# Kernel optimization log

Measured on AMD Instinct MI355X. Metric: run time of the kernel, lower is better.

## Reference

```python
import math
import jax, jax.numpy as jnp
import numpy as np

VOCAB = 50257
HIDDEN = 768
TYPE_VOCAB = 2
MAX_POS = 5000
EPS = 1e-12


def sinusoidal_pe(max_len, dim):
    # matches SinPositionalEncoding: pe[:,0::2]=sin(pos*div), pe[:,1::2]=cos(pos*div)
    position = np.arange(max_len, dtype=np.float32)[:, None]
    div_term = np.exp(np.arange(0, dim, 2, dtype=np.float32) * -(math.log(10000.0) / dim))
    pe = np.zeros((max_len, dim), dtype=np.float32)
    pe[:, 0::2] = np.sin(position * div_term)
    pe[:, 1::2] = np.cos(position * div_term)
    return jnp.asarray(pe)  # [max_len, dim]


def setup_inputs() -> dict:
    key = jax.random.key(0)
    k1, k2, k3, k4, k5 = jax.random.split(key, 5)
    B, N = 8, 4096
    return {
        "input_ids": jax.random.randint(k1, (B, N), 0, VOCAB, dtype=jnp.int64 if jax.config.jax_enable_x64 else jnp.int32),
        "tok_struct_vec": jax.random.randint(k2, (B, N, 3), 0, MAX_POS, dtype=jnp.int32),
        "token_type_ids": jax.random.randint(k3, (B, N), 0, TYPE_VOCAB, dtype=jnp.int32),
        "word_emb": jax.random.normal(k4, (VOCAB, HIDDEN), dtype=jnp.float32) * 0.02,
        "type_emb": jax.random.normal(k5, (TYPE_VOCAB, HIDDEN), dtype=jnp.float32) * 0.02,
        "gamma": jnp.ones((HIDDEN,), dtype=jnp.float32),
        "beta": jnp.zeros((HIDDEN,), dtype=jnp.float32),
    }


def reference(input_ids, tok_struct_vec, token_type_ids, word_emb, type_emb, gamma, beta):
    B, N = input_ids.shape
    pe = sinusoidal_pe(MAX_POS, HIDDEN)  # [max_pos, H]

    words = word_emb[input_ids]                      # [B,N,H] gather
    types = type_emb[token_type_ids]                 # [B,N,H] gather
    pos = jnp.broadcast_to(pe[:N][None], (B, N, HIDDEN))  # pe[:, :n].expand

    # compute_se: vectorized gather of pe rows by structure positions
    para = pe[tok_struct_vec[:, :, 0]]               # [B,N,H]
    sent = pe[tok_struct_vec[:, :, 1]]
    tok = pe[tok_struct_vec[:, :, 2]]
    struct = para + sent + tok                       # tok_se_comb_mode == 'sum'

    emb = words + pos + types + struct
    # BertLayerNorm (eps=1e-12); dropout is identity in eval
    mean = jnp.mean(emb, axis=-1, keepdims=True)
    var = jnp.mean(jnp.square(emb - mean), axis=-1, keepdims=True)
    out = (emb - mean) / jnp.sqrt(var + EPS) * gamma + beta
    return out
```

## Files before the change

kernel.cpp:

```cpp
#include <hip/hip_runtime.h>
#include <hip/hip_fp16.h>
#include <cstdint>
#include <cmath>

#define HIDDEN   768
#define NPAIR    (HIDDEN / 2)
#define SEQ_N    4096
#define LN_EPS   1e-12f
#define N_HI     80
#define N_LO     64
#define NBLK     2048

typedef float    f4v __attribute__((ext_vector_type(4)));
typedef _Float16 h4v __attribute__((ext_vector_type(4)));

__global__ __launch_bounds__(256) void pe_tables_kernel(__half2* __restrict__ T) {
    const int total = (N_HI + N_LO) * NPAIR;
    int idx = blockIdx.x * 256 + threadIdx.x;
    if (idx >= total) return;
    int r = idx / NPAIR;
    int i = idx % NPAIR;
    const float L = logf(10000.0f) / (float)HIDDEN;
    float div = expf(-2.0f * (float)i * L);
    int p = (r < N_HI) ? (r << 6) : (r - N_HI);
    float s, c;
    sincosf((float)p * div, &s, &c);
    T[idx] = __floats2half2_rn(s, c);
}

__device__ __forceinline__ void pe_acc(float4& x, const h4v a, const h4v b) {
    const float sA0 = (float)a.x, cA0 = (float)a.y, sA1 = (float)a.z, cA1 = (float)a.w;
    const float sB0 = (float)b.x, cB0 = (float)b.y, sB1 = (float)b.z, cB1 = (float)b.w;
    x.x = fmaf(sA0, cB0, fmaf(cA0, sB0, x.x));
    x.y = fmaf(cA0, cB0, fmaf(-sA0, sB0, x.y));
    x.z = fmaf(sA1, cB1, fmaf(cA1, sB1, x.z));
    x.w = fmaf(cA1, cB1, fmaf(-sA1, sB1, x.w));
}

__global__ __launch_bounds__(256, 4) void emb_ln_kernel(
    const int*     __restrict__ ids,
    const int*     __restrict__ svec,
    const int*     __restrict__ tt,
    const float*   __restrict__ word_emb,
    const float*   __restrict__ type_emb,
    const float*   __restrict__ gamma,
    const float*   __restrict__ beta,
    const __half2* __restrict__ T,
    float*         __restrict__ out,
    int n_tokens)
{
    const int wave = threadIdx.x >> 6;
    const int lane = threadIdx.x & 63;
    const int nw   = NBLK * 4;
    int tok = blockIdx.x * 4 + wave;
    if (tok >= n_tokens) return;

    int tu = __builtin_amdgcn_readfirstlane(tok);
    int id = ids[tu], ty = tt[tu];
    int p0 = svec[3 * tu], p1 = svec[3 * tu + 1], p2 = svec[3 * tu + 2];

    for (;;) {
        const int n = tu & (SEQ_N - 1);

        const float4* wrow = reinterpret_cast<const float4*>(word_emb + (size_t)id * HIDDEN);
        const float4* trow = reinterpret_cast<const float4*>(type_emb + (size_t)ty * HIDDEN);

        #define T1ROW(p) reinterpret_cast<const h4v*>(T + (size_t)((p) >> 6) * NPAIR)
        #define T2ROW(p) reinterpret_cast<const h4v*>(T + (size_t)(N_HI + ((p) & 63)) * NPAIR)
        const h4v* A0 = T1ROW(n),  *B0 = T2ROW(n);
        const h4v* A1 = T1ROW(p0), *B1 = T2ROW(p0);
        const h4v* A2 = T1ROW(p1), *B2 = T2ROW(p1);
        const h4v* A3 = T1ROW(p2), *B3 = T2ROW(p2);
        #undef T1ROW
        #undef T2ROW

        const int tnext = tu + nw;
        const bool more = tnext < n_tokens;
        int id_n = 0, ty_n = 0, q0 = 0, q1 = 0, q2 = 0;
        if (more) {
            id_n = ids[tnext]; ty_n = tt[tnext];
            q0 = svec[3 * tnext]; q1 = svec[3 * tnext + 1]; q2 = svec[3 * tnext + 2];
        }

        float4 acc[3];
        float s = 0.0f, ss = 0.0f;

        #pragma unroll
        for (int k = 0; k < 3; ++k) {
            const int d4 = lane + 64 * k;

            float4 w = wrow[d4];
            float4 t = trow[d4];
            h4v a0 = A0[d4], b0 = B0[d4];
            h4v a1 = A1[d4], b1 = B1[d4];
            h4v a2 = A2[d4], b2 = B2[d4];
            h4v a3 = A3[d4], b3 = B3[d4];

            float4 x;
            x.x = w.x + t.x; x.y = w.y + t.y; x.z = w.z + t.z; x.w = w.w + t.w;
            pe_acc(x, a0, b0);
            pe_acc(x, a1, b1);
            pe_acc(x, a2, b2);
            pe_acc(x, a3, b3);

            acc[k] = x;
            s  += x.x + x.y + x.z + x.w;
            ss += x.x * x.x + x.y * x.y + x.z * x.z + x.w * x.w;
        }

        #pragma unroll
        for (int off = 1; off < 64; off <<= 1) {
            s  += __shfl_xor(s,  off);
            ss += __shfl_xor(ss, off);
        }

        const float mean = s * (1.0f / (float)HIDDEN);
        const float var  = ss * (1.0f / (float)HIDDEN) - mean * mean;
        const float inv  = rsqrtf(var + LN_EPS);

        const float4* g4 = reinterpret_cast<const float4*>(gamma);
        const float4* b4 = reinterpret_cast<const float4*>(beta);
        float4* orow = reinterpret_cast<float4*>(out + (size_t)tu * HIDDEN);

        #pragma unroll
        for (int k = 0; k < 3; ++k) {
            const int d4 = lane + 64 * k;
            const float4 g = g4[d4];
            const float4 b = b4[d4];
            const float4 x = acc[k];
            float4 r;
            r.x = (x.x - mean) * inv * g.x + b.x;
            r.y = (x.y - mean) * inv * g.y + b.y;
            r.z = (x.z - mean) * inv * g.z + b.z;
            r.w = (x.w - mean) * inv * g.w + b.w;
            orow[d4] = r;
        }

        if (!more) break;
        tu = tnext; id = id_n; ty = ty_n; p0 = q0; p1 = q1; p2 = q2;
    }
}

extern "C" void kernel_launch(void* const* d_in, const int* in_sizes, int n_in,
                              void* d_out, int out_size, void* d_ws, size_t ws_size,
                              hipStream_t stream) {
    const int*   ids      = (const int*)d_in[0];
    const int*   svec     = (const int*)d_in[1];
    const int*   tt       = (const int*)d_in[2];
    const float* word_emb = (const float*)d_in[3];
    const float* type_emb = (const float*)d_in[4];
    const float* gamma    = (const float*)d_in[5];
    const float* beta     = (const float*)d_in[6];
    float*       out      = (float*)d_out;

    const int n_tokens = in_sizes[0];

    __half2* T = (__half2*)d_ws;
    const int total_tab = (N_HI + N_LO) * NPAIR;
    pe_tables_kernel<<<(total_tab + 255) / 256, 256, 0, stream>>>(T);
    emb_ln_kernel<<<NBLK, 256, 0, stream>>>(
        ids, svec, tt, word_emb, type_emb, gamma, beta, T, out, n_tokens);
}
```

Baseline: 51.34 us.

## Software-pipeline word-embedding row loads and use nontemporal output stores

Each wave now prefetches the next token's word-embedding row into registers while it computes the current token, and it fetches the indices two tokens ahead. The aim is to hide the latency of the random gathers from the large word table. The output stores become nontemporal so the streamed result does not pollute the cache. This costs extra VGPRs, which under launch_bounds(256,4) could cause spills or lower occupancy.

```diff
diff --git a/kernel.cpp b/kernel.cpp
--- a/kernel.cpp
+++ b/kernel.cpp
@@ -52,44 +52,59 @@
     const int wave = threadIdx.x >> 6;
     const int lane = threadIdx.x & 63;
     const int nw   = NBLK * 4;
-    int tok = blockIdx.x * 4 + wave;
-    if (tok >= n_tokens) return;
+    int tu = __builtin_amdgcn_readfirstlane(blockIdx.x * 4 + wave);
+    if (tu >= n_tokens) return;
 
-    int tu = __builtin_amdgcn_readfirstlane(tok);
-    int id = ids[tu], ty = tt[tu];
-    int p0 = svec[3 * tu], p1 = svec[3 * tu + 1], p2 = svec[3 * tu + 2];
+    int ty_c = tt[tu];
+    int p0_c = svec[3 * tu], p1_c = svec[3 * tu + 1], p2_c = svec[3 * tu + 2];
+    const int id_c = ids[tu];
+
+    int  tu_n  = tu + nw;
+    bool more1 = tu_n < n_tokens;
+    int id_n = 0, ty_n = 0, p0_n = 0, p1_n = 0, p2_n = 0;
+    if (more1) {
+        id_n = ids[tu_n]; ty_n = tt[tu_n];
+        p0_n = svec[3 * tu_n]; p1_n = svec[3 * tu_n + 1]; p2_n = svec[3 * tu_n + 2];
+    }
+
+    const float4* wr0 = reinterpret_cast<const float4*>(word_emb + (size_t)id_c * HIDDEN);
+    float4 w0 = wr0[lane], w1 = wr0[lane + 64], w2 = wr0[lane + 128];
 
     for (;;) {
+        float4 nw0, nw1, nw2;
+        if (more1) {
+            const float4* wr = reinterpret_cast<const float4*>(word_emb + (size_t)id_n * HIDDEN);
+            nw0 = wr[lane]; nw1 = wr[lane + 64]; nw2 = wr[lane + 128];
+        }
+
+        const int  tu_2  = tu_n + nw;
+        const bool more2 = more1 && (tu_2 < n_tokens);
+        int id_2 = 0, ty_2 = 0, p0_2 = 0, p1_2 = 0, p2_2 = 0;
+        if (more2) {
+            id_2 = ids[tu_2]; ty_2 = tt[tu_2];
+            p0_2 = svec[3 * tu_2]; p1_2 = svec[3 * tu_2 + 1]; p2_2 = svec[3 * tu_2 + 2];
+        }
+
         const int n = tu & (SEQ_N - 1);
-
-        const float4* wrow = reinterpret_cast<const float4*>(word_emb + (size_t)id * HIDDEN);
-        const float4* trow = reinterpret_cast<const float4*>(type_emb + (size_t)ty * HIDDEN);
+        const float4* trow = reinterpret_cast<const float4*>(type_emb + (size_t)ty_c * HIDDEN);
 
         #define T1ROW(p) reinterpret_cast<const h4v*>(T + (size_t)((p) >> 6) * NPAIR)
         #define T2ROW(p) reinterpret_cast<const h4v*>(T + (size_t)(N_HI + ((p) & 63)) * NPAIR)
-        const h4v* A0 = T1ROW(n),  *B0 = T2ROW(n);
-        const h4v* A1 = T1ROW(p0), *B1 = T2ROW(p0);
-        const h4v* A2 = T1ROW(p1), *B2 = T2ROW(p1);
-        const h4v* A3 = T1ROW(p2), *B3 = T2ROW(p2);
+        const h4v* A0 = T1ROW(n),    *B0 = T2ROW(n);
+        const h4v* A1 = T1ROW(p0_c), *B1 = T2ROW(p0_c);
+        const h4v* A2 = T1ROW(p1_c), *B2 = T2ROW(p1_c);
+        const h4v* A3 = T1ROW(p2_c), *B3 = T2ROW(p2_c);
         #undef T1ROW
         #undef T2ROW
 
-        const int tnext = tu + nw;
-        const bool more = tnext < n_tokens;
-        int id_n = 0, ty_n = 0, q0 = 0, q1 = 0, q2 = 0;
-        if (more) {
-            id_n = ids[tnext]; ty_n = tt[tnext];
-            q0 = svec[3 * tnext]; q1 = svec[3 * tnext + 1]; q2 = svec[3 * tnext + 2];
-        }
-
         float4 acc[3];
         float s = 0.0f, ss = 0.0f;
+        const float4 wcur[3] = { w0, w1, w2 };
 
         #pragma unroll
         for (int k = 0; k < 3; ++k) {
             const int d4 = lane + 64 * k;
 
-            float4 w = wrow[d4];
             float4 t = trow[d4];
             h4v a0 = A0[d4], b0 = B0[d4];
             h4v a1 = A1[d4], b1 = B1[d4];
@@ -97,7 +112,8 @@
             h4v a3 = A3[d4], b3 = B3[d4];
 
             float4 x;
-            x.x = w.x + t.x; x.y = w.y + t.y; x.z = w.z + t.z; x.w = w.w + t.w;
+            x.x = wcur[k].x + t.x; x.y = wcur[k].y + t.y;
+            x.z = wcur[k].z + t.z; x.w = wcur[k].w + t.w;
             pe_acc(x, a0, b0);
             pe_acc(x, a1, b1);
             pe_acc(x, a2, b2);
@@ -120,7 +136,7 @@
 
         const float4* g4 = reinterpret_cast<const float4*>(gamma);
         const float4* b4 = reinterpret_cast<const float4*>(beta);
-        float4* orow = reinterpret_cast<float4*>(out + (size_t)tu * HIDDEN);
+        f4v* orow = reinterpret_cast<f4v*>(out + (size_t)tu * HIDDEN);
 
         #pragma unroll
         for (int k = 0; k < 3; ++k) {
@@ -128,16 +144,19 @@
             const float4 g = g4[d4];
             const float4 b = b4[d4];
             const float4 x = acc[k];
-            float4 r;
+            f4v r;
             r.x = (x.x - mean) * inv * g.x + b.x;
             r.y = (x.y - mean) * inv * g.y + b.y;
             r.z = (x.z - mean) * inv * g.z + b.z;
             r.w = (x.w - mean) * inv * g.w + b.w;
-            orow[d4] = r;
+            __builtin_nontemporal_store(r, &orow[d4]);
         }
 
-        if (!more) break;
-        tu = tnext; id = id_n; ty = ty_n; p0 = q0; p1 = q1; p2 = q2;
+        if (!more1) break;
+        tu = tu_n;  ty_c = ty_n;  p0_c = p0_n;  p1_c = p1_n;  p2_c = p2_n;
+        tu_n = tu_2;  more1 = more2;
+        id_n = id_2;  ty_n = ty_2;  p0_n = p0_2;  p1_n = p1_2;  p2_n = p2_2;
+        w0 = nw0;  w1 = nw1;  w2 = nw2;
     }
 }
 
```

Result: no change. 50.91 us (-0.8%).
